# Performance work log

Hardware: AMD Instinct MI355X
Metric: run time of the kernel (lower is better)

## Reference

```python
import jax, jax.numpy as jnp
import numpy as np

BIG_NUMBER = 1000000.0
B, N, H = 8, 256, 128   # batch, nodes, node/hidden feat
E, G = 128, 128         # edge feat, graph feat
MID, OUT = 128, 128
IN_Z = 2 * H


def setup_inputs() -> dict:
    key = jax.random.key(0)
    ks = jax.random.split(key, 20)
    sc = lambda fan_in: 1.0 / np.sqrt(fan_in)
    inp = {
        "node_fts": jax.random.normal(ks[0], (B, N, H), jnp.float32),
        "edge_fts": jax.random.normal(ks[1], (B, N, N, E), jnp.float32),
        "graph_fts": jax.random.normal(ks[2], (B, G), jnp.float32),
        "adj_mat": (jax.random.uniform(ks[3], (B, N, N)) < 0.5).astype(jnp.float32),
        "hidden": jax.random.normal(ks[4], (B, N, H), jnp.float32),
        # linear params, stored [in, out]
        "W1": jax.random.normal(ks[5], (IN_Z, MID), jnp.float32) * sc(IN_Z),
        "b1": jnp.zeros((MID,), jnp.float32),
        "W2": jax.random.normal(ks[6], (IN_Z, MID), jnp.float32) * sc(IN_Z),
        "b2": jnp.zeros((MID,), jnp.float32),
        "We": jax.random.normal(ks[7], (E, MID), jnp.float32) * sc(E),
        "be": jnp.zeros((MID,), jnp.float32),
        "Wg": jax.random.normal(ks[8], (G, MID), jnp.float32) * sc(G),
        "bg": jnp.zeros((MID,), jnp.float32),
        "Wo1": jax.random.normal(ks[9], (IN_Z, OUT), jnp.float32) * sc(IN_Z),
        "bo1": jnp.zeros((OUT,), jnp.float32),
        "Wo2": jax.random.normal(ks[10], (MID, OUT), jnp.float32) * sc(MID),
        "bo2": jnp.zeros((OUT,), jnp.float32),
    }
    return inp


def reference(node_fts, edge_fts, graph_fts, adj_mat, hidden,
              W1, b1, W2, b2, We, be, Wg, bg, Wo1, bo1, Wo2, bo2):
    # z: [b, n, 2h]
    z = jnp.concatenate([node_fts, hidden], axis=-1)
    msg_1 = z @ W1 + b1                       # [b, n, mid]
    msg_2 = z @ W2 + b2                       # [b, n, mid]
    msg_e = edge_fts @ We + be                # [b, n, n, mid]
    msg_g = graph_fts @ Wg + bg               # [b, mid]
    # msgs[b, i, j, :]; reduce over i (senders)
    msgs = (msg_1[:, None, :, :] + msg_2[:, :, None, :]
            + msg_e + msg_g[:, None, None, :])
    maxarg = jnp.where(adj_mat[..., None] > 0, msgs, -BIG_NUMBER)
    msgs_red = jnp.max(maxarg, axis=1)        # [b, n, mid]
    ret = jax.nn.relu((z @ Wo1 + bo1) + (msgs_red @ Wo2 + bo2))
    return ret
```

## Files before the change

### kernel.cpp

```cpp
#include <hip/hip_runtime.h>
#include <stdint.h>
#include <stddef.h>

#define B_   8
#define N_   256
#define H_   128
#define E_   128
#define MIDC 128
#define INZ  256
#define BIGN 1000000.0f

typedef float f32x4 __attribute__((ext_vector_type(4)));
typedef short bf16x8 __attribute__((ext_vector_type(8)));

static __device__ __forceinline__ short f2bf(float f) {
    unsigned u = __builtin_bit_cast(unsigned, f);
    unsigned r = (u + 0x7FFFu + ((u >> 16) & 1u)) >> 16;
    return (short)r;
}

__global__ __launch_bounds__(256) void prep_kernel(
    const float* __restrict__ node, const float* __restrict__ hidden,
    const float* __restrict__ gf,
    const float* __restrict__ W1, const float* __restrict__ b1,
    const float* __restrict__ W2, const float* __restrict__ b2,
    const float* __restrict__ Wg, const float* __restrict__ bg,
    const float* __restrict__ Wo1, const float* __restrict__ bo1,
    const float* __restrict__ We,
    float* __restrict__ msg1, float* __restrict__ m2g,
    float* __restrict__ zo1, unsigned short* __restrict__ weT)
{
    __shared__ float zs[8][INZ];
    const int t  = threadIdx.x;
    const int r0 = blockIdx.x * 8;
    const int b  = r0 >> 8;

    for (int idx = t; idx < 8 * INZ; idx += 256) {
        int r = idx >> 8, k = idx & 255;
        int row = r0 + r;
        zs[r][k] = (k < H_) ? node[(size_t)row * H_ + k]
                            : hidden[(size_t)row * H_ + (k - H_)];
    }
    if (blockIdx.x == 0) {
        for (int e = t; e < 128 * 128; e += 256) {
            int n = e >> 7, k = e & 127;
            weT[(n * 128 + k) ^ ((n & 7) << 3)] =
                (unsigned short)f2bf(We[k * 128 + n]);
        }
    }
    __syncthreads();

    const int col = t & 127;
    const int rg  = t >> 7;
    float a1[4] = {0, 0, 0, 0}, a2[4] = {0, 0, 0, 0}, ao[4] = {0, 0, 0, 0};

#pragma unroll 4
    for (int k = 0; k < INZ; ++k) {
        float w1 = W1[k * 128 + col];
        float w2 = W2[k * 128 + col];
        float wo = Wo1[k * 128 + col];
#pragma unroll
        for (int rr = 0; rr < 4; ++rr) {
            float zv = zs[rg * 4 + rr][k];
            a1[rr] = fmaf(zv, w1, a1[rr]);
            a2[rr] = fmaf(zv, w2, a2[rr]);
            ao[rr] = fmaf(zv, wo, ao[rr]);
        }
    }
    float mg = bg[col];
#pragma unroll 4
    for (int g = 0; g < 128; ++g)
        mg = fmaf(gf[b * 128 + g], Wg[g * 128 + col], mg);

    const float bb1 = b1[col], bb2 = b2[col], bbo = bo1[col];
#pragma unroll
    for (int rr = 0; rr < 4; ++rr) {
        size_t row = (size_t)(r0 + rg * 4 + rr);
        msg1[row * 128 + col] = a1[rr] + bb1;
        m2g[row * 128 + col]  = a2[rr] + bb2 + mg;
        zo1[row * 128 + col]  = ao[rr] + bbo;
    }
}

__global__ __launch_bounds__(256, 2) void pgn_main(
    const float* __restrict__ edge, const float* __restrict__ adj,
    const float* __restrict__ msg1, const float* __restrict__ m2g,
    const float* __restrict__ zo1,
    const unsigned short* __restrict__ weT,
    const float* __restrict__ be, const float* __restrict__ Wo2,
    const float* __restrict__ bo2, float* __restrict__ out)
{
    __shared__ __align__(16) short atile[128 * 128];
    __shared__ __align__(16) float adjt[128];
    __shared__ __align__(16) float redb[512];

    const int t    = threadIdx.x;
    const int lane = t & 63, wid = t >> 6;
    const int wr   = wid >> 1, wn = wid & 1;
    const int hi   = lane >> 4, c15 = lane & 15;
    const int blk  = blockIdx.x;
    const int b    = blk >> 6, jt = blk & 63;
    const int j0   = jt * 4;

    {
        const uint4* src = (const uint4*)weT;
        uint4* dst = (uint4*)atile;
#pragma unroll
        for (int q = 0; q < 8; ++q) dst[t + 256 * q] = src[t + 256 * q];
    }
    __syncthreads();
    bf16x8 bfr[4][4];
#pragma unroll
    for (int n = 0; n < 4; ++n) {
        int rowB = wn * 64 + n * 16 + c15;
#pragma unroll
        for (int ks = 0; ks < 4; ++ks) {
            int a = (rowB * 256 + ks * 64 + hi * 16) ^ ((rowB & 7) << 4);
            bfr[n][ks] = *(const bf16x8*)((const char*)atile + a);
        }
    }
    __syncthreads();

    float rmax[4][4];
#pragma unroll
    for (int n = 0; n < 4; ++n)
#pragma unroll
        for (int rg = 0; rg < 4; ++rg) rmax[n][rg] = -BIGN;

    const int sr = t >> 1, sh = t & 1;
    const size_t istep = (size_t)N_ * E_;
    const size_t base0 = (((size_t)(b * N_) + (sr >> 2)) * N_ + (j0 + (sr & 3))) * E_
                         + (size_t)sh * 64;
    const int wbase = sr * 256 + sh * 128;
    const int swz   = (sr & 7) << 4;

    for (int it = 0; it < 8; ++it) {
        const int i0 = it * 32;
        const float4* src = (const float4*)(edge + base0 + (size_t)i0 * istep);
#pragma unroll
        for (int q = 0; q < 8; ++q) {
            float4 f0 = src[2 * q];
            float4 f1 = src[2 * q + 1];
            bf16x8 s;
            s[0] = f2bf(f0.x); s[1] = f2bf(f0.y); s[2] = f2bf(f0.z); s[3] = f2bf(f0.w);
            s[4] = f2bf(f1.x); s[5] = f2bf(f1.y); s[6] = f2bf(f1.z); s[7] = f2bf(f1.w);
            *(bf16x8*)((char*)atile + ((wbase + q * 16) ^ swz)) = s;
        }
        if (t < 128)
            adjt[t] = adj[(size_t)(b * N_ + i0 + (t >> 2)) * N_ + j0 + (t & 3)];
        __syncthreads();

        f32x4 acc[4][4] = {};
#pragma unroll
        for (int ks = 0; ks < 4; ++ks) {
            bf16x8 af[4];
#pragma unroll
            for (int m = 0; m < 4; ++m) {
                int rowA = wr * 64 + m * 16 + c15;
                int a = (rowA * 256 + ks * 64 + hi * 16) ^ ((rowA & 7) << 4);
                af[m] = *(const bf16x8*)((const char*)atile + a);
            }
#pragma unroll
            for (int m = 0; m < 4; ++m)
#pragma unroll
                for (int n = 0; n < 4; ++n)
                    acc[m][n] = __builtin_amdgcn_mfma_f32_16x16x32_bf16(
                        af[m], bfr[n][ks], acc[m][n], 0, 0, 0);
        }

#pragma unroll
        for (int m = 0; m < 4; ++m) {
            int i_loc = wr * 16 + m * 4 + hi;
            f32x4 am = *(const f32x4*)&adjt[i_loc * 4];
            const float* mp = m2g + (size_t)(b * N_ + i0 + i_loc) * 128 + wn * 64 + c15;
#pragma unroll
            for (int n = 0; n < 4; ++n) {
                float mv = mp[n * 16];
#pragma unroll
                for (int rg = 0; rg < 4; ++rg) {
                    float v = acc[m][n][rg] + mv;
                    v = (am[rg] > 0.0f) ? v : -BIGN;
                    rmax[n][rg] = fmaxf(rmax[n][rg], v);
                }
            }
        }
        __syncthreads();
    }

#pragma unroll
    for (int n = 0; n < 4; ++n)
#pragma unroll
        for (int rg = 0; rg < 4; ++rg) {
            float v = rmax[n][rg];
            v = fmaxf(v, __shfl_xor(v, 16, 64));
            v = fmaxf(v, __shfl_xor(v, 32, 64));
            rmax[n][rg] = v;
        }
    if (wr == 0 && lane < 16) {
#pragma unroll
        for (int n = 0; n < 4; ++n)
#pragma unroll
            for (int rg = 0; rg < 4; ++rg)
                redb[rg * 128 + wn * 64 + n * 16 + c15] = rmax[n][rg];
    }
    __syncthreads();
    if (wr == 1 && lane < 16) {
#pragma unroll
        for (int n = 0; n < 4; ++n)
#pragma unroll
            for (int rg = 0; rg < 4; ++rg) {
                int e = rg * 128 + wn * 64 + n * 16 + c15;
                redb[e] = fmaxf(redb[e], rmax[n][rg]);
            }
    }
    __syncthreads();

    for (int e = t; e < 512; e += 256) {
        int jj = e >> 7, k = e & 127;
        redb[e] += msg1[(size_t)(b * N_ + j0 + jj) * 128 + k] + be[k];
    }
    __syncthreads();

    {
        const int col = t & 127;
        const int jh  = t >> 7;
#pragma unroll
        for (int jx = 0; jx < 2; ++jx) {
            int jj = jh * 2 + jx;
            size_t row = (size_t)(b * N_ + j0 + jj);
            float a = 0.0f;
#pragma unroll 8
            for (int k = 0; k < 128; ++k)
                a = fmaf(redb[jj * 128 + k], Wo2[k * 128 + col], a);
            float o = zo1[row * 128 + col] + bo2[col] + a;
            out[row * 128 + col] = fmaxf(o, 0.0f);
        }
    }
}

extern "C" void kernel_launch(void* const* d_in, const int* in_sizes, int n_in,
                              void* d_out, int out_size, void* d_ws, size_t ws_size,
                              hipStream_t stream) {
    const float* node   = (const float*)d_in[0];
    const float* edge   = (const float*)d_in[1];
    const float* gf     = (const float*)d_in[2];
    const float* adj    = (const float*)d_in[3];
    const float* hidden = (const float*)d_in[4];
    const float* W1  = (const float*)d_in[5];
    const float* b1  = (const float*)d_in[6];
    const float* W2  = (const float*)d_in[7];
    const float* b2  = (const float*)d_in[8];
    const float* We  = (const float*)d_in[9];
    const float* be  = (const float*)d_in[10];
    const float* Wg  = (const float*)d_in[11];
    const float* bg  = (const float*)d_in[12];
    const float* Wo1 = (const float*)d_in[13];
    const float* bo1 = (const float*)d_in[14];
    const float* Wo2 = (const float*)d_in[15];
    const float* bo2 = (const float*)d_in[16];
    float* out = (float*)d_out;

    float* msg1 = (float*)d_ws;
    float* m2g  = msg1 + 2048 * 128;
    float* zo1  = m2g + 2048 * 128;
    unsigned short* weT = (unsigned short*)(zo1 + 2048 * 128);

    hipLaunchKernelGGL(prep_kernel, dim3(256), dim3(256), 0, stream,
                       node, hidden, gf, W1, b1, W2, b2, Wg, bg, Wo1, bo1, We,
                       msg1, m2g, zo1, weT);
    hipLaunchKernelGGL(pgn_main, dim3(512), dim3(256), 0, stream,
                       edge, adj, msg1, m2g, zo1, weT, be, Wo2, bo2, out);
}
```

Baseline: 100.3 us.

## Register-prefetch next edge tile and keep We in a separate LDS buffer

Each iteration now prefetches the next 32-sender edge slice and the matching adjacency values into registers while the MFMA work on the current tile runs, so global load latency overlaps with compute. The We^T tile moves from registers into its own LDS buffer and is re-read for every k-step, which frees 64 VGPRs for the prefetch buffers. m2g loads are issued before the MFMAs, and __syncthreads is replaced with raw s_barrier plus sched_barrier fences. The extra 32 KB of LDS per block and the higher register pressure may cap occupancy below the 2 blocks per CU targeted by launch_bounds.

```diff
diff --git a/kernel.cpp b/kernel.cpp
--- a/kernel.cpp
+++ b/kernel.cpp
@@ -91,6 +91,7 @@
     const float* __restrict__ bo2, float* __restrict__ out)
 {
     __shared__ __align__(16) short atile[128 * 128];
+    __shared__ __align__(16) short wlds[128 * 128];
     __shared__ __align__(16) float adjt[128];
     __shared__ __align__(16) float redb[512];
 
@@ -102,58 +103,79 @@
     const int b    = blk >> 6, jt = blk & 63;
     const int j0   = jt * 4;
 
-    {
-        const uint4* src = (const uint4*)weT;
-        uint4* dst = (uint4*)atile;
-#pragma unroll
-        for (int q = 0; q < 8; ++q) dst[t + 256 * q] = src[t + 256 * q];
-    }
-    __syncthreads();
-    bf16x8 bfr[4][4];
-#pragma unroll
-    for (int n = 0; n < 4; ++n) {
-        int rowB = wn * 64 + n * 16 + c15;
-#pragma unroll
-        for (int ks = 0; ks < 4; ++ks) {
-            int a = (rowB * 256 + ks * 64 + hi * 16) ^ ((rowB & 7) << 4);
-            bfr[n][ks] = *(const bf16x8*)((const char*)atile + a);
-        }
-    }
-    __syncthreads();
-
-    float rmax[4][4];
-#pragma unroll
-    for (int n = 0; n < 4; ++n)
-#pragma unroll
-        for (int rg = 0; rg < 4; ++rg) rmax[n][rg] = -BIGN;
-
     const int sr = t >> 1, sh = t & 1;
-    const size_t istep = (size_t)N_ * E_;
     const size_t base0 = (((size_t)(b * N_) + (sr >> 2)) * N_ + (j0 + (sr & 3))) * E_
                          + (size_t)sh * 64;
     const int wbase = sr * 256 + sh * 128;
     const int swz   = (sr & 7) << 4;
 
+    uint4 wreg[8];
+    {
+        const uint4* wsrc = (const uint4*)weT;
+#pragma unroll
+        for (int q = 0; q < 8; ++q) wreg[q] = wsrc[t + 256 * q];
+    }
+    float4 pf[16];
+    {
+        const float4* s4 = (const float4*)(edge + base0);
+#pragma unroll
+        for (int q = 0; q < 16; ++q) pf[q] = s4[q];
+    }
+    float adjv = 0.0f;
+    if (t < 128)
+        adjv = adj[(size_t)(b * N_ + (t >> 2)) * N_ + j0 + (t & 3)];
+
+    {
+        uint4* wd = (uint4*)wlds;
+#pragma unroll
+        for (int q = 0; q < 8; ++q) wd[t + 256 * q] = wreg[q];
+    }
+    asm volatile("s_waitcnt lgkmcnt(0)" ::: "memory");
+    __builtin_amdgcn_s_barrier();
+    __builtin_amdgcn_sched_barrier(0);
+
+    float rmax[4][4];
+#pragma unroll
+    for (int n = 0; n < 4; ++n)
+#pragma unroll
+        for (int rg = 0; rg < 4; ++rg) rmax[n][rg] = -BIGN;
+
     for (int it = 0; it < 8; ++it) {
-        const int i0 = it * 32;
-        const float4* src = (const float4*)(edge + base0 + (size_t)i0 * istep);
 #pragma unroll
         for (int q = 0; q < 8; ++q) {
-            float4 f0 = src[2 * q];
-            float4 f1 = src[2 * q + 1];
+            float4 f0 = pf[2 * q];
+            float4 f1 = pf[2 * q + 1];
             bf16x8 s;
             s[0] = f2bf(f0.x); s[1] = f2bf(f0.y); s[2] = f2bf(f0.z); s[3] = f2bf(f0.w);
             s[4] = f2bf(f1.x); s[5] = f2bf(f1.y); s[6] = f2bf(f1.z); s[7] = f2bf(f1.w);
             *(bf16x8*)((char*)atile + ((wbase + q * 16) ^ swz)) = s;
         }
-        if (t < 128)
-            adjt[t] = adj[(size_t)(b * N_ + i0 + (t >> 2)) * N_ + j0 + (t & 3)];
-        __syncthreads();
+        if (t < 128) adjt[t] = adjv;
+        asm volatile("s_waitcnt lgkmcnt(0)" ::: "memory");
+        __builtin_amdgcn_s_barrier();
+        __builtin_amdgcn_sched_barrier(0);
+
+        if (it < 7) {
+            const float4* s4 = (const float4*)(edge + base0 + (size_t)(it + 1) * 32 * (N_ * E_));
+#pragma unroll
+            for (int q = 0; q < 16; ++q) pf[q] = s4[q];
+            if (t < 128)
+                adjv = adj[(size_t)(b * N_ + (it + 1) * 32 + (t >> 2)) * N_ + j0 + (t & 3)];
+        }
+
+        float mv[4][4];
+#pragma unroll
+        for (int m = 0; m < 4; ++m) {
+            int i_loc = wr * 16 + m * 4 + hi;
+            const float* mp = m2g + (size_t)(b * N_ + it * 32 + i_loc) * 128 + wn * 64 + c15;
+#pragma unroll
+            for (int n = 0; n < 4; ++n) mv[m][n] = mp[n * 16];
+        }
 
         f32x4 acc[4][4] = {};
 #pragma unroll
         for (int ks = 0; ks < 4; ++ks) {
-            bf16x8 af[4];
+            bf16x8 af[4], bfv[4];
 #pragma unroll
             for (int m = 0; m < 4; ++m) {
                 int rowA = wr * 64 + m * 16 + c15;
@@ -161,30 +183,35 @@
                 af[m] = *(const bf16x8*)((const char*)atile + a);
             }
 #pragma unroll
+            for (int n = 0; n < 4; ++n) {
+                int rowB = wn * 64 + n * 16 + c15;
+                int a = (rowB * 256 + ks * 64 + hi * 16) ^ ((rowB & 7) << 4);
+                bfv[n] = *(const bf16x8*)((const char*)wlds + a);
+            }
+#pragma unroll
             for (int m = 0; m < 4; ++m)
 #pragma unroll
                 for (int n = 0; n < 4; ++n)
                     acc[m][n] = __builtin_amdgcn_mfma_f32_16x16x32_bf16(
-                        af[m], bfr[n][ks], acc[m][n], 0, 0, 0);
+                        af[m], bfv[n], acc[m][n], 0, 0, 0);
         }
 
 #pragma unroll
         for (int m = 0; m < 4; ++m) {
             int i_loc = wr * 16 + m * 4 + hi;
             f32x4 am = *(const f32x4*)&adjt[i_loc * 4];
-            const float* mp = m2g + (size_t)(b * N_ + i0 + i_loc) * 128 + wn * 64 + c15;
 #pragma unroll
             for (int n = 0; n < 4; ++n) {
-                float mv = mp[n * 16];
 #pragma unroll
                 for (int rg = 0; rg < 4; ++rg) {
-                    float v = acc[m][n][rg] + mv;
+                    float v = acc[m][n][rg] + mv[m][n];
                     v = (am[rg] > 0.0f) ? v : -BIGN;
                     rmax[n][rg] = fmaxf(rmax[n][rg], v);
                 }
             }
         }
-        __syncthreads();
+        __builtin_amdgcn_s_barrier();
+        __builtin_amdgcn_sched_barrier(0);
     }
 
 #pragma unroll
```

New measurement: 115.5 us. +15.2%, slower.

## Split sender reduction across blocks, add finish kernel, shrink edge tiles

Applied to the files above, without the earlier changes.

The main kernel now splits the sender axis across up to two blocks per receiver tile and writes partial max reductions to workspace. A new finish kernel combines the partials and applies the output projection. Edge tiles shrink to 16 senders per iteration with all loads issued before conversion, and weights stay in LDS instead of registers to allow 3 blocks per CU. The prep kernel uses twice as many blocks and distributes the We transpose across 8 blocks. The intent is more parallelism and occupancy for the bandwidth-bound edge stream, at the cost of an extra launch and partial-result traffic.

```diff
diff --git a/kernel.cpp b/kernel.cpp
--- a/kernel.cpp
+++ b/kernel.cpp
@@ -1,4 +1,5 @@
 #include <hip/hip_runtime.h>
+#include <hip/hip_bf16.h>
 #include <stdint.h>
 #include <stddef.h>
 
@@ -6,17 +7,16 @@
 #define N_   256
 #define H_   128
 #define E_   128
-#define MIDC 128
 #define INZ  256
 #define BIGN 1000000.0f
 
 typedef float f32x4 __attribute__((ext_vector_type(4)));
 typedef short bf16x8 __attribute__((ext_vector_type(8)));
 
-static __device__ __forceinline__ short f2bf(float f) {
-    unsigned u = __builtin_bit_cast(unsigned, f);
-    unsigned r = (u + 0x7FFFu + ((u >> 16) & 1u)) >> 16;
-    return (short)r;
+static __device__ __forceinline__ unsigned cvt2(float a, float b) {
+    unsigned short ra = __builtin_bit_cast(unsigned short, __float2bfloat16(a));
+    unsigned short rb = __builtin_bit_cast(unsigned short, __float2bfloat16(b));
+    return (unsigned)ra | ((unsigned)rb << 16);
 }
 
 __global__ __launch_bounds__(256) void prep_kernel(
@@ -30,29 +30,31 @@
     float* __restrict__ msg1, float* __restrict__ m2g,
     float* __restrict__ zo1, unsigned short* __restrict__ weT)
 {
-    __shared__ float zs[8][INZ];
+    __shared__ float zs[4][INZ];
     const int t  = threadIdx.x;
-    const int r0 = blockIdx.x * 8;
+    const int r0 = blockIdx.x * 4;
     const int b  = r0 >> 8;
 
-    for (int idx = t; idx < 8 * INZ; idx += 256) {
+    for (int idx = t; idx < 4 * INZ; idx += 256) {
         int r = idx >> 8, k = idx & 255;
         int row = r0 + r;
         zs[r][k] = (k < H_) ? node[(size_t)row * H_ + k]
                             : hidden[(size_t)row * H_ + (k - H_)];
     }
-    if (blockIdx.x == 0) {
-        for (int e = t; e < 128 * 128; e += 256) {
+    if (blockIdx.x < 8) {
+        int e0 = blockIdx.x * 2048;
+        for (int e = e0 + t; e < e0 + 2048; e += 256) {
             int n = e >> 7, k = e & 127;
             weT[(n * 128 + k) ^ ((n & 7) << 3)] =
-                (unsigned short)f2bf(We[k * 128 + n]);
+                (unsigned short)__builtin_bit_cast(unsigned short,
+                    __float2bfloat16(We[k * 128 + n]));
         }
     }
     __syncthreads();
 
     const int col = t & 127;
     const int rg  = t >> 7;
-    float a1[4] = {0, 0, 0, 0}, a2[4] = {0, 0, 0, 0}, ao[4] = {0, 0, 0, 0};
+    float a1[2] = {0, 0}, a2[2] = {0, 0}, ao[2] = {0, 0};
 
 #pragma unroll 4
     for (int k = 0; k < INZ; ++k) {
@@ -60,8 +62,8 @@
         float w2 = W2[k * 128 + col];
         float wo = Wo1[k * 128 + col];
 #pragma unroll
-        for (int rr = 0; rr < 4; ++rr) {
-            float zv = zs[rg * 4 + rr][k];
+        for (int rr = 0; rr < 2; ++rr) {
+            float zv = zs[rg * 2 + rr][k];
             a1[rr] = fmaf(zv, w1, a1[rr]);
             a2[rr] = fmaf(zv, w2, a2[rr]);
             ao[rr] = fmaf(zv, wo, ao[rr]);
@@ -74,117 +76,124 @@
 
     const float bb1 = b1[col], bb2 = b2[col], bbo = bo1[col];
 #pragma unroll
-    for (int rr = 0; rr < 4; ++rr) {
-        size_t row = (size_t)(r0 + rg * 4 + rr);
+    for (int rr = 0; rr < 2; ++rr) {
+        size_t row = (size_t)(r0 + rg * 2 + rr);
         msg1[row * 128 + col] = a1[rr] + bb1;
         m2g[row * 128 + col]  = a2[rr] + bb2 + mg;
         zo1[row * 128 + col]  = ao[rr] + bbo;
     }
 }
 
-__global__ __launch_bounds__(256, 2) void pgn_main(
+__global__ __launch_bounds__(256, 3) void pgn_main(
     const float* __restrict__ edge, const float* __restrict__ adj,
-    const float* __restrict__ msg1, const float* __restrict__ m2g,
-    const float* __restrict__ zo1,
+    const float* __restrict__ m2g,
     const unsigned short* __restrict__ weT,
-    const float* __restrict__ be, const float* __restrict__ Wo2,
-    const float* __restrict__ bo2, float* __restrict__ out)
+    float* __restrict__ redp, int nsplit)
 {
-    __shared__ __align__(16) short atile[128 * 128];
-    __shared__ __align__(16) float adjt[128];
-    __shared__ __align__(16) float redb[512];
+    __shared__ __align__(16) short atile[64 * 128];
+    __shared__ __align__(16) short wlds[128 * 128];
 
     const int t    = threadIdx.x;
     const int lane = t & 63, wid = t >> 6;
     const int wr   = wid >> 1, wn = wid & 1;
     const int hi   = lane >> 4, c15 = lane & 15;
     const int blk  = blockIdx.x;
-    const int b    = blk >> 6, jt = blk & 63;
+    const int ih   = blk % nsplit;
+    const int jblk = blk / nsplit;
+    const int b    = jblk >> 6, jt = jblk & 63;
     const int j0   = jt * 4;
+    const int irange = N_ / nsplit;
+    const int ibase  = ih * irange;
+    const int ntiles = irange >> 4;
 
     {
-        const uint4* src = (const uint4*)weT;
-        uint4* dst = (uint4*)atile;
-#pragma unroll
-        for (int q = 0; q < 8; ++q) dst[t + 256 * q] = src[t + 256 * q];
-    }
-    __syncthreads();
-    bf16x8 bfr[4][4];
-#pragma unroll
-    for (int n = 0; n < 4; ++n) {
-        int rowB = wn * 64 + n * 16 + c15;
+        const uint4* wsrc = (const uint4*)weT;
+        uint4* wd = (uint4*)wlds;
+#pragma unroll
+        for (int q = 0; q < 8; ++q) wd[t + 256 * q] = wsrc[t + 256 * q];
+    }
+
+    const int th    = t >> 7;
+    const int jj_s  = (t >> 5) & 3;
+    const int f4c   = t & 31;
+    const size_t gbase0 = (((size_t)(b * N_) + ibase + th) * N_ + (j0 + jj_s)) * E_
+                          + (size_t)f4c * 4;
+    const size_t qstep  = (size_t)2 * N_ * E_;
+    const int r0c = 4 * th + jj_s;
+    char* lbase = (char*)atile + r0c * 256 + ((f4c * 8) ^ (r0c << 4));
+
+    float rmax[4][4];
+#pragma unroll
+    for (int n = 0; n < 4; ++n)
+#pragma unroll
+        for (int rg = 0; rg < 4; ++rg) rmax[n][rg] = -BIGN;
+
+    __syncthreads();
+
+    for (int it = 0; it < ntiles; ++it) {
+        const float* gsrc = edge + gbase0 + (size_t)it * 16 * N_ * E_;
+        float4 f[8];
+#pragma unroll
+        for (int q = 0; q < 8; ++q)
+            f[q] = *(const float4*)(gsrc + q * qstep);
+#pragma unroll
+        for (int q = 0; q < 8; ++q) {
+            uint2 s;
+            s.x = cvt2(f[q].x, f[q].y);
+            s.y = cvt2(f[q].z, f[q].w);
+            *(uint2*)(lbase + q * 2048) = s;
+        }
+        __syncthreads();
+
+        float am[2][4], mv[2][4];
+#pragma unroll
+        for (int m = 0; m < 2; ++m) {
+            int ig = ibase + it * 16 + wr * 8 + m * 4 + hi;
+            f32x4 a4 = *(const f32x4*)(adj + (size_t)(b * N_ + ig) * N_ + j0);
+#pragma unroll
+            for (int rg = 0; rg < 4; ++rg) am[m][rg] = a4[rg];
+            const float* mp = m2g + (size_t)(b * N_ + ig) * 128 + wn * 64 + c15;
+#pragma unroll
+            for (int n = 0; n < 4; ++n) mv[m][n] = mp[n * 16];
+        }
+
+        f32x4 acc[2][4] = {};
 #pragma unroll
         for (int ks = 0; ks < 4; ++ks) {
-            int a = (rowB * 256 + ks * 64 + hi * 16) ^ ((rowB & 7) << 4);
-            bfr[n][ks] = *(const bf16x8*)((const char*)atile + a);
-        }
-    }
-    __syncthreads();
-
-    float rmax[4][4];
-#pragma unroll
-    for (int n = 0; n < 4; ++n)
-#pragma unroll
-        for (int rg = 0; rg < 4; ++rg) rmax[n][rg] = -BIGN;
-
-    const int sr = t >> 1, sh = t & 1;
-    const size_t istep = (size_t)N_ * E_;
-    const size_t base0 = (((size_t)(b * N_) + (sr >> 2)) * N_ + (j0 + (sr & 3))) * E_
-                         + (size_t)sh * 64;
-    const int wbase = sr * 256 + sh * 128;
-    const int swz   = (sr & 7) << 4;
-
-    for (int it = 0; it < 8; ++it) {
-        const int i0 = it * 32;
-        const float4* src = (const float4*)(edge + base0 + (size_t)i0 * istep);
-#pragma unroll
-        for (int q = 0; q < 8; ++q) {
-            float4 f0 = src[2 * q];
-            float4 f1 = src[2 * q + 1];
-            bf16x8 s;
-            s[0] = f2bf(f0.x); s[1] = f2bf(f0.y); s[2] = f2bf(f0.z); s[3] = f2bf(f0.w);
-            s[4] = f2bf(f1.x); s[5] = f2bf(f1.y); s[6] = f2bf(f1.z); s[7] = f2bf(f1.w);
-            *(bf16x8*)((char*)atile + ((wbase + q * 16) ^ swz)) = s;
-        }
-        if (t < 128)
-            adjt[t] = adj[(size_t)(b * N_ + i0 + (t >> 2)) * N_ + j0 + (t & 3)];
-        __syncthreads();
-
-        f32x4 acc[4][4] = {};
-#pragma unroll
-        for (int ks = 0; ks < 4; ++ks) {
-            bf16x8 af[4];
-#pragma unroll
-            for (int m = 0; m < 4; ++m) {
-                int rowA = wr * 64 + m * 16 + c15;
+            bf16x8 af[2], bfv[4];
+#pragma unroll
+            for (int m = 0; m < 2; ++m) {
+                int rowA = wr * 32 + m * 16 + c15;
                 int a = (rowA * 256 + ks * 64 + hi * 16) ^ ((rowA & 7) << 4);
                 af[m] = *(const bf16x8*)((const char*)atile + a);
             }
 #pragma unroll
-            for (int m = 0; m < 4; ++m)
+            for (int n = 0; n < 4; ++n) {
+                int rowB = wn * 64 + n * 16 + c15;
+                int a = (rowB * 256 + ks * 64 + hi * 16) ^ ((rowB & 7) << 4);
+                bfv[n] = *(const bf16x8*)((const char*)wlds + a);
+            }
+#pragma unroll
+            for (int m = 0; m < 2; ++m)
 #pragma unroll
                 for (int n = 0; n < 4; ++n)
                     acc[m][n] = __builtin_amdgcn_mfma_f32_16x16x32_bf16(
-                        af[m], bfr[n][ks], acc[m][n], 0, 0, 0);
-        }
-
-#pragma unroll
-        for (int m = 0; m < 4; ++m) {
-            int i_loc = wr * 16 + m * 4 + hi;
-            f32x4 am = *(const f32x4*)&adjt[i_loc * 4];
-            const float* mp = m2g + (size_t)(b * N_ + i0 + i_loc) * 128 + wn * 64 + c15;
+                        af[m], bfv[n], acc[m][n], 0, 0, 0);
+        }
+        __syncthreads();
+
+#pragma unroll
+        for (int m = 0; m < 2; ++m) {
 #pragma unroll
             for (int n = 0; n < 4; ++n) {
-                float mv = mp[n * 16];
 #pragma unroll
                 for (int rg = 0; rg < 4; ++rg) {
-                    float v = acc[m][n][rg] + mv;
-                    v = (am[rg] > 0.0f) ? v : -BIGN;
+                    float v = acc[m][n][rg] + mv[m][n];
+                    v = (am[m][rg] > 0.0f) ? v : -BIGN;
                     rmax[n][rg] = fmaxf(rmax[n][rg], v);
                 }
             }
         }
-        __syncthreads();
     }
 
 #pragma unroll
@@ -196,6 +205,7 @@
             v = fmaxf(v, __shfl_xor(v, 32, 64));
             rmax[n][rg] = v;
         }
+    float* redb = (float*)atile;
     if (wr == 0 && lane < 16) {
 #pragma unroll
         for (int n = 0; n < 4; ++n)
@@ -214,27 +224,44 @@
             }
     }
     __syncthreads();
-
-    for (int e = t; e < 512; e += 256) {
-        int jj = e >> 7, k = e & 127;
-        redb[e] += msg1[(size_t)(b * N_ + j0 + jj) * 128 + k] + be[k];
-    }
-    __syncthreads();
-
-    {
-        const int col = t & 127;
-        const int jh  = t >> 7;
-#pragma unroll
-        for (int jx = 0; jx < 2; ++jx) {
-            int jj = jh * 2 + jx;
-            size_t row = (size_t)(b * N_ + j0 + jj);
-            float a = 0.0f;
+#pragma unroll
+    for (int e = t; e < 512; e += 256)
+        redp[(size_t)blk * 512 + e] = redb[e];
+}
+
+__global__ __launch_bounds__(256) void finish_kernel(
+    const float* __restrict__ redp, const float* __restrict__ msg1,
+    const float* __restrict__ zo1, const float* __restrict__ be,
+    const float* __restrict__ Wo2, const float* __restrict__ bo2,
+    float* __restrict__ out, int nsplit)
+{
+    __shared__ float rb[8][128];
+    const int t  = threadIdx.x;
+    const int r0 = blockIdx.x * 8;
+
+    for (int idx = t; idx < 1024; idx += 256) {
+        int rr = idx >> 7, k = idx & 127;
+        int r = r0 + rr;
+        int jblk = r >> 2, jj = r & 3;
+        float v = -BIGN - 1.0f;
+        for (int p = 0; p < nsplit; ++p)
+            v = fmaxf(v, redp[(size_t)(jblk * nsplit + p) * 512 + jj * 128 + k]);
+        rb[rr][k] = v + msg1[(size_t)r * 128 + k] + be[k];
+    }
+    __syncthreads();
+
+    const int col = t & 127;
+    const int half = t >> 7;
+#pragma unroll
+    for (int rx = 0; rx < 4; ++rx) {
+        int rr = half * 4 + rx;
+        size_t row = (size_t)(r0 + rr);
+        float a = 0.0f;
 #pragma unroll 8
-            for (int k = 0; k < 128; ++k)
-                a = fmaf(redb[jj * 128 + k], Wo2[k * 128 + col], a);
-            float o = zo1[row * 128 + col] + bo2[col] + a;
-            out[row * 128 + col] = fmaxf(o, 0.0f);
-        }
+        for (int k = 0; k < 128; ++k)
+            a = fmaf(rb[rr][k], Wo2[k * 128 + col], a);
+        float o = zo1[row * 128 + col] + bo2[col] + a;
+        out[row * 128 + col] = fmaxf(o, 0.0f);
     }
 }
 
@@ -264,10 +291,16 @@
     float* m2g  = msg1 + 2048 * 128;
     float* zo1  = m2g + 2048 * 128;
     unsigned short* weT = (unsigned short*)(zo1 + 2048 * 128);
-
-    hipLaunchKernelGGL(prep_kernel, dim3(256), dim3(256), 0, stream,
+    float* redp = (float*)((char*)weT + 128 * 128 * sizeof(unsigned short));
+
+    const size_t base_bytes = 3u * 1048576u + 32768u;
+    int nsplit = (ws_size >= base_bytes + 2u * 1048576u) ? 2 : 1;
+
+    hipLaunchKernelGGL(prep_kernel, dim3(512), dim3(256), 0, stream,
                        node, hidden, gf, W1, b1, W2, b2, Wg, bg, Wo1, bo1, We,
                        msg1, m2g, zo1, weT);
-    hipLaunchKernelGGL(pgn_main, dim3(512), dim3(256), 0, stream,
-                       edge, adj, msg1, m2g, zo1, weT, be, Wo2, bo2, out);
-}
+    hipLaunchKernelGGL(pgn_main, dim3(512 * nsplit), dim3(256), 0, stream,
+                       edge, adj, m2g, weT, redp, nsplit);
+    hipLaunchKernelGGL(finish_kernel, dim3(256), dim3(256), 0, stream,
+                       redp, msg1, zo1, be, Wo2, bo2, out, nsplit);
+}
```

Measured after the change: 110.0 us. 9.7% more time.
